# Optimization experiments

Hardware: AMD Instinct MI355X
Metric: run time of the kernel (lower is better)

## Reference

```python
import jax, jax.numpy as jnp
import numpy as np
from math import sqrt


def _build_transitions(dim):
    # Upper-triangular (i<=j) pairs in the same row-major order as the torch loop.
    iu0, iu1 = np.triu_indices(dim)
    n_mono = len(iu0)
    idx = np.arange(n_mono)
    M = np.zeros((dim, dim), dtype=np.int32)
    M[iu0, iu1] = idx
    M[iu1, iu0] = idx
    coef_trans = np.full((n_mono, 1), sqrt(2.0), dtype=np.float32)
    coef_trans[idx[iu0 == iu1]] = 1.0  # diagonal coefficients stay scale 1
    return iu0, iu1, M.reshape(-1), coef_trans


def setup_inputs() -> dict:
    key = jax.random.key(0)
    k1, k2, k3, k4 = jax.random.split(key, 4)
    dim, n_quadrics, B = 512, 64, 2048
    n_mono = dim * (dim - 1) // 2 + dim  # 131328
    points = jax.random.normal(k1, (B, dim), dtype=jnp.float32)
    # orthogonal-ish init is only an init detail; random normal keeps math identical
    q_coefs = jax.random.normal(k2, (n_mono, n_quadrics), dtype=jnp.float32) / np.sqrt(n_mono)
    l_coefs = 2.0 * jax.random.uniform(k3, (dim, n_quadrics), dtype=jnp.float32) - 1.0
    free_coefs = 2.0 * jax.random.uniform(k4, (1, n_quadrics), dtype=jnp.float32) - 1.0
    return {"points": points, "q_coefs": q_coefs, "l_coefs": l_coefs, "free_coefs": free_coefs}


def reference(points, q_coefs, l_coefs, free_coefs):
    B, dim = points.shape
    nq = q_coefs.shape[1]
    iu0, iu1, inds_trans, coef_trans_np = _build_transitions(dim)
    coef_trans = jnp.asarray(coef_trans_np)

    # quadratic monomials: q[b, k] = p[b, i_k] * p[b, j_k]  (upper-tri order)
    q = points[:, iu0] * points[:, iu1]  # (B, n_mono)

    coefs = q_coefs * coef_trans  # (n_mono, nq) real coefficients

    # values of quadrics at points
    values = jnp.abs(q @ coefs + points @ l_coefs + free_coefs)  # (B, nq)

    # symmetric full matrices gathered from flat coefficient vector
    m_full = coefs[inds_trans].reshape(dim, dim, nq)  # (dim, dim, nq)
    dm = (jnp.eye(dim, dtype=points.dtype) + 1.0)[:, :, None]  # 2 on diag, ... wait: eye+ones -> 2 diag, 1 off
    m_scaled = m_full * dm

    # gradients: grad[b, k, e] = sum_d p[b, d] * m_scaled[d, e, k] + l_coefs[e, k]
    q_grad = jnp.einsum("bd,dek->bke", points, m_scaled) + l_coefs.T[None, :, :]  # (B, nq, dim)
    grad = jnp.sum(q_grad * q_grad, axis=2)  # (B, nq)

    norm = jnp.linalg.norm(q_coefs, axis=0)  # (nq,)
    scores = (jnp.sqrt(grad / 4.0 + values * norm) - jnp.sqrt(grad) / 2.0) / norm
    return scores
```

## Files before the change

### kernel.cpp

```cpp
#include <hip/hip_runtime.h>

#define DIM 512
#define NQ 64
#define BATCH 2048

typedef __bf16  bf16x8  __attribute__((ext_vector_type(8)));
typedef float   floatx4 __attribute__((ext_vector_type(4)));

static __device__ inline unsigned short f2bf(float f) {
    unsigned int u = __float_as_uint(f);
    return (unsigned short)((u + 0x7fffu + ((u >> 16) & 1u)) >> 16);
}
static __device__ inline float bf2f(unsigned short h) {
    return __uint_as_float((unsigned int)h << 16);
}
static __device__ inline unsigned int pack2(float a, float b) {
    return (unsigned)f2bf(a) | ((unsigned)f2bf(b) << 16);
}

__global__ void hsq_pack_kernel(const float* __restrict__ pts,
                                unsigned short* __restrict__ Pb) {
    const int i8 = blockIdx.x * 256 + threadIdx.x;
    const float4 v1 = *(const float4*)(pts + (size_t)i8 * 8);
    const float4 v2 = *(const float4*)(pts + (size_t)i8 * 8 + 4);
    uint4 wv;
    wv.x = pack2(v1.x, v1.y); wv.y = pack2(v1.z, v1.w);
    wv.z = pack2(v2.x, v2.y); wv.w = pack2(v2.z, v2.w);
    *(uint4*)(Pb + (size_t)i8 * 8) = wv;
}

__global__ __launch_bounds__(256, 4)
void hsq_expand_kernel(const float* __restrict__ qc,
                       unsigned short* __restrict__ W,
                       float* __restrict__ npart) {
    const int e    = blockIdx.x;
    const int dblk = blockIdx.y;
    const int pb   = blockIdx.y * 512 + blockIdx.x;
    const int wid  = threadIdx.x >> 6;
    const int k    = threadIdx.x & 63;
    const int d0   = dblk * 128 + wid * 32;

    __shared__ unsigned short tv[64 * 136];
    __shared__ float part[4][64];

    float v[32];
#pragma unroll
    for (int s = 0; s < 32; ++s) {
        const int d = d0 + s;
        const int i = d < e ? d : e;
        const int j = d < e ? e : d;
        const int idx = i * DIM - ((i * (i - 1)) >> 1) + (j - i);
        v[s] = qc[(size_t)idx * NQ + k];
    }

    float nacc = 0.0f;
#pragma unroll
    for (int s = 0; s < 32; ++s)
        if (d0 + s >= e) nacc += v[s] * v[s];

#pragma unroll
    for (int t = 0; t < 4; ++t) {
        float sc[8];
#pragma unroll
        for (int q = 0; q < 8; ++q) {
            const int d = d0 + t * 8 + q;
            sc[q] = v[t * 8 + q] * ((d == e) ? 2.0f : 1.41421356237309515f);
        }
        uint4 w;
        w.x = pack2(sc[0], sc[1]); w.y = pack2(sc[2], sc[3]);
        w.z = pack2(sc[4], sc[5]); w.w = pack2(sc[6], sc[7]);
        *(uint4*)&tv[k * 136 + wid * 32 + t * 8] = w;
    }
    part[wid][k] = nacc;
    __syncthreads();

#pragma unroll
    for (int r = 0; r < 4; ++r) {
        const int kk = r * 16 + (threadIdx.x >> 4);
        const int u  = threadIdx.x & 15;
        const uint4 w = *(const uint4*)&tv[kk * 136 + u * 8];
        *(uint4*)(W + ((size_t)(kk * DIM + e)) * DIM + dblk * 128 + u * 8) = w;
    }
    if (threadIdx.x < 64) {
        npart[(size_t)k * 2048 + pb] =
            part[0][k] + part[1][k] + part[2][k] + part[3][k];
    }
}

__global__ void hsq_normred_kernel(const float* __restrict__ npart,
                                   float* __restrict__ norm2) {
    const int t = threadIdx.x;
    const int k = blockIdx.x * 8 + (t >> 5);
    const int q = t & 31;
    const float4* src = (const float4*)(npart + (size_t)k * 2048 + q * 64);
    float s = 0.f;
#pragma unroll
    for (int i = 0; i < 16; ++i) {
        const float4 v = src[i];
        s += v.x + v.y + v.z + v.w;
    }
#pragma unroll
    for (int off = 1; off < 32; off <<= 1) s += __shfl_xor(s, off);
    if (q == 0) norm2[k] = s;
}

__global__ __launch_bounds__(256, 2)
void hsq_gemm_kernel(const unsigned short* __restrict__ Pb,
                     const unsigned short* __restrict__ W,
                     const float* __restrict__ l_coefs,
                     float2* __restrict__ part) {
    const int bid = blockIdx.x;
    const int xcd = bid & 7;
    const int loc = bid >> 3;
    const int k   = xcd * 8 + (loc >> 6);
    const int rem = loc & 63;
    const int eb  = rem >> 4;
    const int m0  = (rem & 15) * 128;

    const int tid   = threadIdx.x;
    const int w     = tid >> 6;
    const int lane  = tid & 63;
    const int mhalf = w >> 1, nhalf = w & 1;
    const int c     = lane & 15;
    const int quad  = lane >> 4;

    __shared__ unsigned short Ab[2][128 * 64];
    __shared__ unsigned short Bb[2][128 * 64];
    __shared__ float red[2][128][2];

    const unsigned short* Wk = W + (size_t)k * DIM * DIM + (size_t)eb * 128 * DIM;

#define STAGE(buf_, it_) do {                                                   \
    const int rl_ = (lane >> 3);                                                \
    const int s_  = lane & 7;                                                   \
    _Pragma("unroll")                                                           \
    for (int i_ = 0; i_ < 4; ++i_) {                                            \
        const int row_ = w * 32 + i_ * 8 + rl_;                                 \
        const int gch_ = s_ ^ (row_ & 7);                                       \
        __builtin_amdgcn_global_load_lds(                                       \
            (const __attribute__((address_space(1))) unsigned int*)             \
                (Pb + (size_t)(m0 + row_) * DIM + (it_) * 64 + gch_ * 8),       \
            (__attribute__((address_space(3))) unsigned int*)                   \
                &Ab[buf_][(w * 32 + i_ * 8) * 64], 16, 0, 0);                   \
        __builtin_amdgcn_global_load_lds(                                       \
            (const __attribute__((address_space(1))) unsigned int*)             \
                (Wk + (size_t)row_ * DIM + (it_) * 64 + gch_ * 8),              \
            (__attribute__((address_space(3))) unsigned int*)                   \
                &Bb[buf_][(w * 32 + i_ * 8) * 64], 16, 0, 0);                   \
    }                                                                           \
} while (0)

    floatx4 acc[4][4];
#pragma unroll
    for (int mt = 0; mt < 4; ++mt)
#pragma unroll
        for (int nt = 0; nt < 4; ++nt)
            acc[mt][nt] = (floatx4){0.f, 0.f, 0.f, 0.f};

    float lcv[4];
#pragma unroll
    for (int nt = 0; nt < 4; ++nt)
        lcv[nt] = l_coefs[(eb * 128 + nhalf * 64 + nt * 16 + c) * NQ + k];

    float pf[4][4][4];
    const int hit = 2 * eb + nhalf;

    STAGE(0, 0);
    __syncthreads();

    for (int it = 0; it < 8; ++it) {
        const int buf = it & 1;
        if (it < 7) STAGE(buf ^ 1, it + 1);

        if (it == hit) {
#pragma unroll
            for (int mt = 0; mt < 4; ++mt)
#pragma unroll
                for (int r = 0; r < 4; ++r) {
                    const int row = mhalf * 64 + mt * 16 + quad * 4 + r;
#pragma unroll
                    for (int nt = 0; nt < 4; ++nt) {
                        const int slot = (nt * 2 + (c >> 3)) ^ (row & 7);
                        pf[mt][r][nt] = bf2f(Ab[buf][row * 64 + slot * 8 + (c & 7)]);
                    }
                }
        }

#pragma unroll
        for (int ks = 0; ks < 2; ++ks) {
            bf16x8 af[4], bfr[4];
#pragma unroll
            for (int mt = 0; mt < 4; ++mt) {
                const int row = mhalf * 64 + mt * 16 + c;
                const int slot = (ks * 4 + quad) ^ (row & 7);
                af[mt] = *(const bf16x8*)&Ab[buf][row * 64 + slot * 8];
            }
#pragma unroll
            for (int nt = 0; nt < 4; ++nt) {
                const int er = nhalf * 64 + nt * 16 + c;
                const int slot = (ks * 4 + quad) ^ (er & 7);
                bfr[nt] = *(const bf16x8*)&Bb[buf][er * 64 + slot * 8];
            }
#pragma unroll
            for (int mt = 0; mt < 4; ++mt)
#pragma unroll
                for (int nt = 0; nt < 4; ++nt)
                    acc[mt][nt] = __builtin_amdgcn_mfma_f32_16x16x32_bf16(
                        af[mt], bfr[nt], acc[mt][nt], 0, 0, 0);
        }
        __syncthreads();
    }
#undef STAGE

#pragma unroll
    for (int mt = 0; mt < 4; ++mt)
#pragma unroll
        for (int r = 0; r < 4; ++r) {
            float pv = 0.f, pg = 0.f;
#pragma unroll
            for (int nt = 0; nt < 4; ++nt) {
                const float g = acc[mt][nt][r];
                const float l = lcv[nt];
                pv += pf[mt][r][nt] * (0.5f * g + l);
                const float gq = g + l;
                pg += gq * gq;
            }
#pragma unroll
            for (int off = 1; off < 16; off <<= 1) {
                pv += __shfl_xor(pv, off);
                pg += __shfl_xor(pg, off);
            }
            if (c == 0) {
                const int row = mhalf * 64 + mt * 16 + quad * 4 + r;
                red[nhalf][row][0] = pv;
                red[nhalf][row][1] = pg;
            }
        }
    __syncthreads();

    if (tid < 128) {
        const float pv = red[0][tid][0] + red[1][tid][0];
        const float pg = red[0][tid][1] + red[1][tid][1];
        part[((size_t)(eb * NQ + k)) * BATCH + m0 + tid] = make_float2(pv, pg);
    }
}

__global__ void hsq_final_kernel(const float2* __restrict__ part,
                                 const float* __restrict__ norm2,
                                 const float* __restrict__ free_coefs,
                                 float* __restrict__ out) {
    const int k = blockIdx.x;
    const float nrm = sqrtf(norm2[k]);
    const float fc  = free_coefs[k];
#pragma unroll
    for (int i = 0; i < 8; ++i) {
        const int b = i * 256 + threadIdx.x;
        float pv = 0.f, pg = 0.f;
#pragma unroll
        for (int eb = 0; eb < 4; ++eb) {
            const float2 t = part[((size_t)(eb * NQ + k)) * BATCH + b];
            pv += t.x; pg += t.y;
        }
        const float vals = fabsf(pv + fc);
        out[(size_t)b * NQ + k] = (sqrtf(0.25f * pg + vals * nrm) - 0.5f * sqrtf(pg)) / nrm;
    }
}

extern "C" void kernel_launch(void* const* d_in, const int* in_sizes, int n_in,
                              void* d_out, int out_size, void* d_ws, size_t ws_size,
                              hipStream_t stream) {
    const float* points     = (const float*)d_in[0];
    const float* q_coefs    = (const float*)d_in[1];
    const float* l_coefs    = (const float*)d_in[2];
    const float* free_coefs = (const float*)d_in[3];
    float* out = (float*)d_out;

    char* ws = (char*)d_ws;
    unsigned short* W  = (unsigned short*)ws;
    unsigned short* Pb = (unsigned short*)(ws + 33554432);
    float2*         part  = (float2*)(ws + 35651584);
    float*          npart = (float*)(ws + 39845888);
    float*          norm2 = (float*)(ws + 40370176);

    hsq_pack_kernel<<<dim3(BATCH * DIM / 8 / 256), 256, 0, stream>>>(points, Pb);
    hsq_expand_kernel<<<dim3(DIM, 4), 256, 0, stream>>>(q_coefs, W, npart);
    hsq_normred_kernel<<<dim3(8), 256, 0, stream>>>(npart, norm2);
    hsq_gemm_kernel<<<dim3(NQ * 64), 256, 0, stream>>>(Pb, W, l_coefs, part);
    hsq_final_kernel<<<dim3(NQ), 256, 0, stream>>>(part, norm2, free_coefs, out);
}
```

Measured before the change: 219.0 us.

## Halve GEMM K-tile to 32 for higher occupancy and fold norm reduction into final

The GEMM K-step per stage drops from 64 to 32, which halves LDS use per block. The LDS swizzle is reworked to match, and launch bounds are raised from 2 to 4 blocks per SM so more waves can hide latency. The point-value extraction now captures packed bf16 pairs over two iterations, which trims register use. The separate norm-reduction kernel is removed and its work folded into the final kernel, saving one launch. The cost is twice as many loop iterations and barriers, plus tighter register limits that could cause spills.

```diff
diff --git a/kernel.cpp b/kernel.cpp
--- a/kernel.cpp
+++ b/kernel.cpp
@@ -87,24 +87,7 @@
     }
 }
 
-__global__ void hsq_normred_kernel(const float* __restrict__ npart,
-                                   float* __restrict__ norm2) {
-    const int t = threadIdx.x;
-    const int k = blockIdx.x * 8 + (t >> 5);
-    const int q = t & 31;
-    const float4* src = (const float4*)(npart + (size_t)k * 2048 + q * 64);
-    float s = 0.f;
-#pragma unroll
-    for (int i = 0; i < 16; ++i) {
-        const float4 v = src[i];
-        s += v.x + v.y + v.z + v.w;
-    }
-#pragma unroll
-    for (int off = 1; off < 32; off <<= 1) s += __shfl_xor(s, off);
-    if (q == 0) norm2[k] = s;
-}
-
-__global__ __launch_bounds__(256, 2)
+__global__ __launch_bounds__(256, 4)
 void hsq_gemm_kernel(const unsigned short* __restrict__ Pb,
                      const unsigned short* __restrict__ W,
                      const float* __restrict__ l_coefs,
@@ -124,29 +107,29 @@
     const int c     = lane & 15;
     const int quad  = lane >> 4;
 
-    __shared__ unsigned short Ab[2][128 * 64];
-    __shared__ unsigned short Bb[2][128 * 64];
+    __shared__ unsigned short Ab[2][128 * 32];
+    __shared__ unsigned short Bb[2][128 * 32];
     __shared__ float red[2][128][2];
 
     const unsigned short* Wk = W + (size_t)k * DIM * DIM + (size_t)eb * 128 * DIM;
 
 #define STAGE(buf_, it_) do {                                                   \
-    const int rl_ = (lane >> 3);                                                \
-    const int s_  = lane & 7;                                                   \
+    const int lr_  = lane >> 2;                                                 \
+    const int gch_ = (lane & 3) ^ ((lane >> 3) & 3);                            \
     _Pragma("unroll")                                                           \
-    for (int i_ = 0; i_ < 4; ++i_) {                                            \
-        const int row_ = w * 32 + i_ * 8 + rl_;                                 \
-        const int gch_ = s_ ^ (row_ & 7);                                       \
+    for (int i_ = 0; i_ < 2; ++i_) {                                            \
+        const int rb_  = w * 32 + i_ * 16;                                      \
+        const int row_ = rb_ + lr_;                                             \
         __builtin_amdgcn_global_load_lds(                                       \
             (const __attribute__((address_space(1))) unsigned int*)             \
-                (Pb + (size_t)(m0 + row_) * DIM + (it_) * 64 + gch_ * 8),       \
+                (Pb + (size_t)(m0 + row_) * DIM + (it_) * 32 + gch_ * 8),       \
             (__attribute__((address_space(3))) unsigned int*)                   \
-                &Ab[buf_][(w * 32 + i_ * 8) * 64], 16, 0, 0);                   \
+                &Ab[buf_][rb_ * 32], 16, 0, 0);                                 \
         __builtin_amdgcn_global_load_lds(                                       \
             (const __attribute__((address_space(1))) unsigned int*)             \
-                (Wk + (size_t)row_ * DIM + (it_) * 64 + gch_ * 8),              \
+                (Wk + (size_t)row_ * DIM + (it_) * 32 + gch_ * 8),              \
             (__attribute__((address_space(3))) unsigned int*)                   \
-                &Bb[buf_][(w * 32 + i_ * 8) * 64], 16, 0, 0);                   \
+                &Bb[buf_][rb_ * 32], 16, 0, 0);                                 \
     }                                                                           \
 } while (0)
 
@@ -162,52 +145,52 @@
     for (int nt = 0; nt < 4; ++nt)
         lcv[nt] = l_coefs[(eb * 128 + nhalf * 64 + nt * 16 + c) * NQ + k];
 
-    float pf[4][4][4];
-    const int hit = 2 * eb + nhalf;
+    unsigned int pf[4][4][2];
+    const int hit_a = 4 * eb + 2 * nhalf;
+    const int hit_b = hit_a + 1;
 
     STAGE(0, 0);
     __syncthreads();
 
-    for (int it = 0; it < 8; ++it) {
+#pragma unroll 2
+    for (int it = 0; it < 16; ++it) {
         const int buf = it & 1;
-        if (it < 7) STAGE(buf ^ 1, it + 1);
-
-        if (it == hit) {
+        if (it < 15) STAGE(buf ^ 1, it + 1);
+
+        if (it == hit_a || it == hit_b) {
+            const int hi = (it == hit_b);
+            const int c7 = c & 7, ch0 = c >> 3;
 #pragma unroll
             for (int mt = 0; mt < 4; ++mt)
 #pragma unroll
                 for (int r = 0; r < 4; ++r) {
                     const int row = mhalf * 64 + mt * 16 + quad * 4 + r;
-#pragma unroll
-                    for (int nt = 0; nt < 4; ++nt) {
-                        const int slot = (nt * 2 + (c >> 3)) ^ (row & 7);
-                        pf[mt][r][nt] = bf2f(Ab[buf][row * 64 + slot * 8 + (c & 7)]);
-                    }
+                    const int sw  = (row >> 1) & 3;
+                    const unsigned short u0 = Ab[buf][row * 32 + ((ch0 ^ sw)) * 8 + c7];
+                    const unsigned short u1 = Ab[buf][row * 32 + (((2 | ch0) ^ sw)) * 8 + c7];
+                    pf[mt][r][hi] = (unsigned)u0 | ((unsigned)u1 << 16);
                 }
         }
 
-#pragma unroll
-        for (int ks = 0; ks < 2; ++ks) {
-            bf16x8 af[4], bfr[4];
-#pragma unroll
-            for (int mt = 0; mt < 4; ++mt) {
-                const int row = mhalf * 64 + mt * 16 + c;
-                const int slot = (ks * 4 + quad) ^ (row & 7);
-                af[mt] = *(const bf16x8*)&Ab[buf][row * 64 + slot * 8];
-            }
-#pragma unroll
-            for (int nt = 0; nt < 4; ++nt) {
-                const int er = nhalf * 64 + nt * 16 + c;
-                const int slot = (ks * 4 + quad) ^ (er & 7);
-                bfr[nt] = *(const bf16x8*)&Bb[buf][er * 64 + slot * 8];
-            }
-#pragma unroll
-            for (int mt = 0; mt < 4; ++mt)
-#pragma unroll
-                for (int nt = 0; nt < 4; ++nt)
-                    acc[mt][nt] = __builtin_amdgcn_mfma_f32_16x16x32_bf16(
-                        af[mt], bfr[nt], acc[mt][nt], 0, 0, 0);
-        }
+        bf16x8 af[4], bfr[4];
+#pragma unroll
+        for (int mt = 0; mt < 4; ++mt) {
+            const int row  = mhalf * 64 + mt * 16 + c;
+            const int slot = quad ^ ((row >> 1) & 3);
+            af[mt] = *(const bf16x8*)&Ab[buf][row * 32 + slot * 8];
+        }
+#pragma unroll
+        for (int nt = 0; nt < 4; ++nt) {
+            const int er   = nhalf * 64 + nt * 16 + c;
+            const int slot = quad ^ ((er >> 1) & 3);
+            bfr[nt] = *(const bf16x8*)&Bb[buf][er * 32 + slot * 8];
+        }
+#pragma unroll
+        for (int mt = 0; mt < 4; ++mt)
+#pragma unroll
+            for (int nt = 0; nt < 4; ++nt)
+                acc[mt][nt] = __builtin_amdgcn_mfma_f32_16x16x32_bf16(
+                    af[mt], bfr[nt], acc[mt][nt], 0, 0, 0);
         __syncthreads();
     }
 #undef STAGE
@@ -216,12 +199,17 @@
     for (int mt = 0; mt < 4; ++mt)
 #pragma unroll
         for (int r = 0; r < 4; ++r) {
+            const float p0 = bf2f((unsigned short)(pf[mt][r][0] & 0xffff));
+            const float p1 = bf2f((unsigned short)(pf[mt][r][0] >> 16));
+            const float p2 = bf2f((unsigned short)(pf[mt][r][1] & 0xffff));
+            const float p3 = bf2f((unsigned short)(pf[mt][r][1] >> 16));
+            const float pp[4] = {p0, p1, p2, p3};
             float pv = 0.f, pg = 0.f;
 #pragma unroll
             for (int nt = 0; nt < 4; ++nt) {
                 const float g = acc[mt][nt][r];
                 const float l = lcv[nt];
-                pv += pf[mt][r][nt] * (0.5f * g + l);
+                pv += pp[nt] * (0.5f * g + l);
                 const float gq = g + l;
                 pg += gq * gq;
             }
@@ -246,23 +234,34 @@
 }
 
 __global__ void hsq_final_kernel(const float2* __restrict__ part,
-                                 const float* __restrict__ norm2,
+                                 const float* __restrict__ npart,
                                  const float* __restrict__ free_coefs,
                                  float* __restrict__ out) {
     const int k = blockIdx.x;
-    const float nrm = sqrtf(norm2[k]);
+    const int t = threadIdx.x;
+    __shared__ float ws[4];
+
+    const float4* src = (const float4*)(npart + (size_t)k * 2048);
+    const float4 a = src[t * 2], b = src[t * 2 + 1];
+    float s = a.x + a.y + a.z + a.w + b.x + b.y + b.z + b.w;
+#pragma unroll
+    for (int off = 1; off < 64; off <<= 1) s += __shfl_xor(s, off);
+    if ((t & 63) == 0) ws[t >> 6] = s;
+    __syncthreads();
+    const float nrm = sqrtf(ws[0] + ws[1] + ws[2] + ws[3]);
     const float fc  = free_coefs[k];
+
 #pragma unroll
     for (int i = 0; i < 8; ++i) {
-        const int b = i * 256 + threadIdx.x;
+        const int bidx = i * 256 + t;
         float pv = 0.f, pg = 0.f;
 #pragma unroll
         for (int eb = 0; eb < 4; ++eb) {
-            const float2 t = part[((size_t)(eb * NQ + k)) * BATCH + b];
-            pv += t.x; pg += t.y;
+            const float2 p = part[((size_t)(eb * NQ + k)) * BATCH + bidx];
+            pv += p.x; pg += p.y;
         }
         const float vals = fabsf(pv + fc);
-        out[(size_t)b * NQ + k] = (sqrtf(0.25f * pg + vals * nrm) - 0.5f * sqrtf(pg)) / nrm;
+        out[(size_t)bidx * NQ + k] = (sqrtf(0.25f * pg + vals * nrm) - 0.5f * sqrtf(pg)) / nrm;
     }
 }
 
@@ -280,11 +279,9 @@
     unsigned short* Pb = (unsigned short*)(ws + 33554432);
     float2*         part  = (float2*)(ws + 35651584);
     float*          npart = (float*)(ws + 39845888);
-    float*          norm2 = (float*)(ws + 40370176);
 
     hsq_pack_kernel<<<dim3(BATCH * DIM / 8 / 256), 256, 0, stream>>>(points, Pb);
     hsq_expand_kernel<<<dim3(DIM, 4), 256, 0, stream>>>(q_coefs, W, npart);
-    hsq_normred_kernel<<<dim3(8), 256, 0, stream>>>(npart, norm2);
     hsq_gemm_kernel<<<dim3(NQ * 64), 256, 0, stream>>>(Pb, W, l_coefs, part);
-    hsq_final_kernel<<<dim3(NQ), 256, 0, stream>>>(part, norm2, free_coefs, out);
-}
+    hsq_final_kernel<<<dim3(NQ), 256, 0, stream>>>(part, npart, free_coefs, out);
+}
```

Measured after the change: 226.5 us. 3.5% more time.
